# Kernel optimization log

Measured on AMD Instinct MI355X. Metric: run time of the kernel, lower is better.

Reference implementation:

```python
import jax, jax.numpy as jnp
from jax import lax
import numpy as np

T = 65536   # seq_len (one long utterance)
C = 8       # n_cgs (contour generators in graph)
F = 10      # n_features + n_context
H = 64      # GRU hidden size
NIN = 4     # rnn_inputs=None -> x_module[:, 1:5]
NOUT = 1    # n_output


def setup_inputs() -> dict:
    key = jax.random.key(0)
    ks = jax.random.split(key, 9)
    x = jax.random.normal(ks[0], (T, F, C), jnp.float32)
    cg_masks = jnp.ones((T, C), jnp.int32)
    contour_starts = jax.random.randint(ks[1], (T, C), 0, 2, jnp.int32)
    # first timestep of each cg must start a contour (original loop only
    # produces output from the first start onward)
    contour_starts = contour_starts.at[0].set(1)
    s = 1.0 / np.sqrt(H)
    u = lambda k, shp: jax.random.uniform(k, shp, jnp.float32, -s, s)
    W_ih = u(ks[2], (C, 3 * H, NIN))
    W_hh = u(ks[3], (C, 3 * H, H))
    b_ih = u(ks[4], (C, 3 * H))
    b_hh = u(ks[5], (C, 3 * H))
    W_out = u(ks[6], (C, NOUT, H))
    b_out = u(ks[7], (C, NOUT))
    return {"x": x, "cg_masks": cg_masks, "contour_starts": contour_starts,
            "W_ih": W_ih, "W_hh": W_hh, "b_ih": b_ih, "b_hh": b_hh,
            "W_out": W_out, "b_out": b_out}


def reference(x, cg_masks, contour_starts, W_ih, W_hh, b_ih, b_hh, W_out, b_out):
    # x: (T, F, C); select rnn input features 1:5 for every contour generator
    x4 = x[:, 1:5, :]                                   # (T, 4, C)
    # precompute input-to-hidden gates for all cgs at once: (T, C, 3H)
    gx = jnp.einsum('tfc,cgf->tcg', x4, W_ih) + b_ih
    starts = contour_starts == 1                        # (T, C) bool

    def step(h, inp):
        gx_t, start_t = inp                             # (C, 3H), (C,)
        # ragged segment boundary -> reset hidden state (h_module = None)
        h = jnp.where(start_t[:, None], jnp.zeros_like(h), h)
        gh = jnp.einsum('cgh,ch->cg', W_hh, h) + b_hh   # (C, 3H)
        r = jax.nn.sigmoid(gx_t[:, :H] + gh[:, :H])
        z = jax.nn.sigmoid(gx_t[:, H:2 * H] + gh[:, H:2 * H])
        n = jnp.tanh(gx_t[:, 2 * H:] + r * gh[:, 2 * H:])
        h_new = (1.0 - z) * n + z * h
        return h_new, h_new

    h0 = jnp.zeros((C, H), x.dtype)
    _, hs = lax.scan(step, h0, (gx, starts))            # hs: (T, C, H)
    out = jnp.einsum('tch,coh->tco', hs, W_out) + b_out  # (T, C, NOUT)
    # scatter-add of each segment's y_rnn into y; with all-ones masks the
    # segments tile [0, T) so this is the masked sum over contour generators
    active = (cg_masks == 1).astype(out.dtype)[..., None]  # (T, C, 1)
    y = jnp.sum(out * active, axis=1)                   # (T, NOUT)
    return y
```

## Files before the change

kernel.cpp:

```cpp
#include <hip/hip_runtime.h>

#define T_LEN 65536
#define C_CH 8
#define CLEN 16
#define NB 16
#define WIN (CLEN * NB)
#define NBLK 2048
#define SCANW 6
#define MAXB 32

typedef short bf16x8 __attribute__((ext_vector_type(8)));
typedef float f32x4 __attribute__((ext_vector_type(4)));
typedef unsigned int uint;
typedef uint u32x4 __attribute__((ext_vector_type(4)));
typedef unsigned long long u64;

#define MFMA32 __builtin_amdgcn_mfma_f32_16x16x32_bf16

#define SC_RZ 1.4426950408889634f
#define SC_N  2.8853900817779268f

__device__ __forceinline__ uint f2bf(float f) {
    uint u = __float_as_uint(f);
    return (u + 0x7FFFu + ((u >> 16) & 1u)) >> 16;
}
__device__ __forceinline__ uint pk(float a, float b) {
    return f2bf(a) | (f2bf(b) << 16);
}
__device__ __forceinline__ uint cvtpk(float lo, float hi) {
    uint r;
    asm("v_cvt_pk_bf16_f32 %0, %1, %2" : "=v"(r) : "v"(lo), "v"(hi));
    return r;
}
__device__ __forceinline__ float expneg(float x) { return __builtin_amdgcn_exp2f(-x); }
__device__ __forceinline__ bf16x8 mk8(uint a, uint b, uint c, uint d) {
    union { uint u[4]; bf16x8 v; } x;
    x.u[0] = a; x.u[1] = b; x.u[2] = c; x.u[3] = d;
    return x.v;
}
__device__ __forceinline__ bf16x8 q2b(u32x4 q) {
    union { u32x4 q; bf16x8 b; } u; u.q = q; return u.b;
}
__device__ __forceinline__ float rcpf(float v) { return __builtin_amdgcn_rcpf(v); }

__global__ __launch_bounds__(64, 2) void gru_mfma(
    const float* __restrict__ x,
    const int*   __restrict__ cg,
    const int*   __restrict__ cs,
    const float* __restrict__ W_ih,
    const float* __restrict__ W_hh,
    const float* __restrict__ b_ih,
    const float* __restrict__ b_hh,
    const float* __restrict__ W_out,
    const float* __restrict__ b_out,
    float* __restrict__ y)
{
    __shared__ u64 stw[SCANW], acw[SCANW];
    __shared__ int sb[NB + 1];
    __shared__ float yw[NB][MAXB + 1];
    __shared__ uint2 bxl[MAXB][NB];

    const int lane = threadIdx.x;
    const int l15 = lane & 15, l4 = lane >> 4;
    const int slot = blockIdx.x & 7;
    const int c    = (blockIdx.x >> 3) & 7;
    const int whi  = blockIdx.x >> 6;
    const int w    = whi * 8 + slot;
    const int RB   = w * WIN;

    for (int rr = 0; rr < SCANW; ++rr) {
        int t = RB + rr * 64 + lane;
        int sv = 0, av = 0;
        if (t < T_LEN) { sv = cs[t * C_CH + c]; av = cg[t * C_CH + c]; }
        u64 m1 = __ballot(sv == 1);
        u64 m2 = __ballot(av == 1);
        if (lane == 0) { stw[rr] = m1; acw[rr] = m2; }
    }
    __syncthreads();

    if (lane <= NB) {
        int rel = lane * CLEN;
        int q = rel >> 6, r0 = rel & 63;
        u64 m = stw[q] >> r0;
        int pos = -1;
        if (m) pos = rel + __ffsll(m) - 1;
        else {
            for (int q2 = q + 1; q2 < SCANW; ++q2)
                if (stw[q2]) { pos = (q2 << 6) + __ffsll(stw[q2]) - 1; break; }
        }
        int Sa;
        if (pos >= 0) Sa = RB + pos;
        else {
            int t = RB + SCANW * 64;
            while (t < T_LEN && cs[t * C_CH + c] != 1) ++t;
            Sa = t;
        }
        sb[lane] = min(Sa, T_LEN);
    }
    __syncthreads();

    const int S = sb[l15];
    const int len = sb[l15 + 1] - S;
    int Lmax = len;
#pragma unroll
    for (int o = 1; o < 16; o <<= 1) Lmax = max(Lmax, __shfl_xor(Lmax, o));

    const float* Wc = W_hh + c * 192 * 64;
    u32x4 AhA[12][2];
#pragma unroll
    for (int tm = 0; tm < 12; ++tm) {
        const float sc = (tm < 8) ? SC_RZ : SC_N;
#pragma unroll
        for (int kt = 0; kt < 2; ++kt) {
            const float* p = Wc + (16 * tm + l15) * 64 + 32 * kt + 4 * l4;
            float4 a = *(const float4*)p;
            float4 b = *(const float4*)(p + 16);
            AhA[tm][kt] = (u32x4){ pk(a.x * sc, a.y * sc), pk(a.z * sc, a.w * sc),
                                   pk(b.x * sc, b.y * sc), pk(b.z * sc, b.w * sc) };
            asm volatile("" : "+a"(AhA[tm][kt]));
        }
    }
    u32x4 WoA[2];
#pragma unroll
    for (int kt = 0; kt < 2; ++kt) {
        uint d0 = 0, d1 = 0, d2 = 0, d3 = 0;
        if (l15 == 0) {
            const float* wp = W_out + c * 64 + 32 * kt + 4 * l4;
            d0 = pk(wp[0], wp[1]);  d1 = pk(wp[2], wp[3]);
            d2 = pk(wp[16], wp[17]); d3 = pk(wp[18], wp[19]);
        }
        WoA[kt] = (u32x4){ d0, d1, d2, d3 };
        asm volatile("" : "+a"(WoA[kt]));
    }

    uint Axd[12][2];
#pragma unroll
    for (int tm = 0; tm < 12; ++tm) {
        const float sc = (tm < 8) ? SC_RZ : SC_N;
        int row = 16 * tm + l15;
        uint d0 = 0, d1 = 0;
        if (l4 == 0) {
            float4 wi4 = *(const float4*)(W_ih + (c * 192 + row) * 4);
            d0 = pk(wi4.x * sc, wi4.y * sc);
            d1 = pk(wi4.z * sc, wi4.w * sc);
        } else if (l4 == 1) {
            float bias = (tm < 8) ? (b_ih[c * 192 + row] + b_hh[c * 192 + row]) * SC_RZ
                                  : b_ih[c * 192 + row] * SC_N;
            d0 = f2bf(bias);
        }
        Axd[tm][0] = d0; Axd[tm][1] = d1;
    }
    f32x4 bhn4[4];
#pragma unroll
    for (int tn = 0; tn < 4; ++tn) {
        float4 v = *(const float4*)(b_hh + c * 192 + 128 + 16 * tn + 4 * l4);
        bhn4[tn] = (f32x4){v.x * SC_N, v.y * SC_N, v.z * SC_N, v.w * SC_N};
    }
    const float bo = b_out[c];

    uint B0[4], B1[4];
#pragma unroll
    for (int i = 0; i < 4; ++i) { B0[i] = 0u; B1[i] = 0u; }
    const uint bx_c0 = (l4 == 1) ? 0x00003F80u : 0u;
    const f32x4 z4 = {0.f, 0.f, 0.f, 0.f};

    for (int s0 = 0; s0 < Lmax; s0 += MAXB) {
        const int Lb = min(MAXB, Lmax - s0);

        const int npair = Lb * NB;
        for (int p = lane; p < npair; p += 64) {
            int s = p >> 4;
            int t = min(sb[p & 15] + s0 + s, T_LEN - 1);
            const float* xp = x + (size_t)t * 80 + 8 + c;
            bxl[s][p & 15] = make_uint2(pk(xp[0], xp[8]), pk(xp[16], xp[24]));
        }
        int off = (S - RB) + s0;
        int q = off >> 6, r0 = off & 63;
        u64 w0s = (q < SCANW) ? stw[q] : 0ull;
        u64 w1s = (q + 1 < SCANW) ? stw[q + 1] : 0ull;
        u64 ms = (w0s >> r0) | (r0 ? (w1s << (64 - r0)) : 0ull);
        __syncthreads();

        for (int s = 0; s < Lb; ++s) {
            const bool rst = (ms >> s) & 1;
#pragma unroll
            for (int i = 0; i < 4; ++i) {
                B0[i] = rst ? 0u : B0[i];
                B1[i] = rst ? 0u : B1[i];
            }

            uint2 bx = bxl[s][l15];
            const bf16x8 Bx  = mk8((lane < 16) ? bx.x : bx_c0,
                                   (lane < 16) ? bx.y : 0u, 0u, 0u);
            const bf16x8 Bh0 = mk8(B0[0], B0[1], B0[2], B0[3]);
            const bf16x8 Bh1 = mk8(B1[0], B1[1], B1[2], B1[3]);

            uint nB[8];
#pragma unroll
            for (int tm = 0; tm < 4; ++tm) {
                const int tz = tm + 4, tn = tm + 8;
                f32x4 ar = MFMA32(mk8(Axd[tm][0], Axd[tm][1], 0u, 0u), Bx, z4, 0, 0, 0);
                ar = MFMA32(q2b(AhA[tm][0]), Bh0, ar, 0, 0, 0);
                ar = MFMA32(q2b(AhA[tm][1]), Bh1, ar, 0, 0, 0);
                f32x4 az = MFMA32(mk8(Axd[tz][0], Axd[tz][1], 0u, 0u), Bx, z4, 0, 0, 0);
                az = MFMA32(q2b(AhA[tz][0]), Bh0, az, 0, 0, 0);
                az = MFMA32(q2b(AhA[tz][1]), Bh1, az, 0, 0, 0);
                f32x4 gx = MFMA32(mk8(Axd[tn][0], Axd[tn][1], 0u, 0u), Bx, z4, 0, 0, 0);
                f32x4 gh = MFMA32(q2b(AhA[tn][0]), Bh0, bhn4[tm], 0, 0, 0);
                gh = MFMA32(q2b(AhA[tn][1]), Bh1, gh, 0, 0, 0);

                float hv[4];
#pragma unroll
                for (int i = 0; i < 4; ++i) {
                    float rr = rcpf(1.f + expneg(ar[i]));
                    float zz = rcpf(1.f + expneg(az[i]));
                    float np2 = fmaf(rr, gh[i], gx[i]);
                    float nn = fmaf(2.f, rcpf(1.f + expneg(np2)), -1.f);
                    const uint bd = (tm < 2) ? B0[2 * (tm & 1) + (i >> 1)]
                                             : B1[2 * (tm & 1) + (i >> 1)];
                    const float hold = __uint_as_float((i & 1) ? (bd & 0xFFFF0000u)
                                                               : (bd << 16));
                    float hh = fmaf(zz, hold - nn, nn);
                    hv[i] = hh;
                }
                nB[2 * tm]     = cvtpk(hv[0], hv[1]);
                nB[2 * tm + 1] = cvtpk(hv[2], hv[3]);
            }
            B0[0] = nB[0]; B0[1] = nB[1]; B0[2] = nB[2]; B0[3] = nB[3];
            B1[0] = nB[4]; B1[1] = nB[5]; B1[2] = nB[6]; B1[3] = nB[7];

            const bf16x8 Bh0n = mk8(B0[0], B0[1], B0[2], B0[3]);
            const bf16x8 Bh1n = mk8(B1[0], B1[1], B1[2], B1[3]);
            f32x4 y4 = MFMA32(q2b(WoA[0]), Bh0n, z4, 0, 0, 0);
            y4 = MFMA32(q2b(WoA[1]), Bh1n, y4, 0, 0, 0);
            if (lane < 16 && (s0 + s) < len) yw[lane][s] = y4[0];
        }
        __syncthreads();

        for (int b = 0; b < NB; ++b) {
            int Sb = sb[b];
            int lenb = sb[b + 1] - Sb;
            int sg = s0 + lane;
            if (lane < Lb && sg < lenb) {
                int offa = (Sb - RB) + sg;
                int qa = offa >> 6;
                bool act;
                if (qa < SCANW) act = (acw[qa] >> (offa & 63)) & 1;
                else            act = cg[(Sb + sg) * C_CH + c] == 1;
                if (act) atomicAdd(&y[Sb + sg], yw[b][lane] + bo);
            }
        }
        __syncthreads();
    }
}

extern "C" void kernel_launch(void* const* d_in, const int* in_sizes, int n_in,
                              void* d_out, int out_size, void* d_ws, size_t ws_size,
                              hipStream_t stream) {
    const float* x     = (const float*)d_in[0];
    const int*   cg    = (const int*)  d_in[1];
    const int*   cs    = (const int*)  d_in[2];
    const float* W_ih  = (const float*)d_in[3];
    const float* W_hh  = (const float*)d_in[4];
    const float* b_ih  = (const float*)d_in[5];
    const float* b_hh  = (const float*)d_in[6];
    const float* W_out = (const float*)d_in[7];
    const float* b_out = (const float*)d_in[8];
    float* y = (float*)d_out;

    hipMemsetAsync(y, 0, (size_t)out_size * sizeof(float), stream);
    gru_mfma<<<NBLK, 64, 0, stream>>>(x, cg, cs, W_ih, W_hh, b_ih, b_hh,
                                      W_out, b_out, y);
}
```

Measured before the change: 81.42 us.

## Split MFMA accumulation chains, prefetch next-step input, raise wave priority

The recurrent step's three dependent MFMA chains per gate are each split into two independent partial accumulators that are summed in VALU, which shortens the serial MFMA dependency on the critical path. The next timestep's packed input is loaded from LDS one iteration ahead, so its latency is off the step's critical path. The step body is also wrapped in s_setprio so these waves get issue priority over others on the same SIMD. In exchange there are extra VALU adds and live registers, and rounding order changes slightly.

```diff
diff --git a/kernel.cpp b/kernel.cpp
--- a/kernel.cpp
+++ b/kernel.cpp
@@ -181,7 +181,13 @@
         u64 ms = (w0s >> r0) | (r0 ? (w1s << (64 - r0)) : 0ull);
         __syncthreads();
 
+        uint2 bxn = bxl[0][l15];
+
         for (int s = 0; s < Lb; ++s) {
+            __builtin_amdgcn_s_setprio(1);
+            const uint2 bxc = bxn;
+            if (s + 1 < Lb) bxn = bxl[s + 1][l15];
+
             const bool rst = (ms >> s) & 1;
 #pragma unroll
             for (int i = 0; i < 4; ++i) {
@@ -189,9 +195,8 @@
                 B1[i] = rst ? 0u : B1[i];
             }
 
-            uint2 bx = bxl[s][l15];
-            const bf16x8 Bx  = mk8((lane < 16) ? bx.x : bx_c0,
-                                   (lane < 16) ? bx.y : 0u, 0u, 0u);
+            const bf16x8 Bx  = mk8((lane < 16) ? bxc.x : bx_c0,
+                                   (lane < 16) ? bxc.y : 0u, 0u, 0u);
             const bf16x8 Bh0 = mk8(B0[0], B0[1], B0[2], B0[3]);
             const bf16x8 Bh1 = mk8(B1[0], B1[1], B1[2], B1[3]);
 
@@ -199,22 +204,22 @@
 #pragma unroll
             for (int tm = 0; tm < 4; ++tm) {
                 const int tz = tm + 4, tn = tm + 8;
-                f32x4 ar = MFMA32(mk8(Axd[tm][0], Axd[tm][1], 0u, 0u), Bx, z4, 0, 0, 0);
-                ar = MFMA32(q2b(AhA[tm][0]), Bh0, ar, 0, 0, 0);
-                ar = MFMA32(q2b(AhA[tm][1]), Bh1, ar, 0, 0, 0);
-                f32x4 az = MFMA32(mk8(Axd[tz][0], Axd[tz][1], 0u, 0u), Bx, z4, 0, 0, 0);
-                az = MFMA32(q2b(AhA[tz][0]), Bh0, az, 0, 0, 0);
-                az = MFMA32(q2b(AhA[tz][1]), Bh1, az, 0, 0, 0);
-                f32x4 gx = MFMA32(mk8(Axd[tn][0], Axd[tn][1], 0u, 0u), Bx, z4, 0, 0, 0);
-                f32x4 gh = MFMA32(q2b(AhA[tn][0]), Bh0, bhn4[tm], 0, 0, 0);
-                gh = MFMA32(q2b(AhA[tn][1]), Bh1, gh, 0, 0, 0);
+                f32x4 arx = MFMA32(mk8(Axd[tm][0], Axd[tm][1], 0u, 0u), Bx, z4, 0, 0, 0);
+                f32x4 aru = MFMA32(q2b(AhA[tm][0]), Bh0, arx, 0, 0, 0);
+                f32x4 arv = MFMA32(q2b(AhA[tm][1]), Bh1, z4, 0, 0, 0);
+                f32x4 azx = MFMA32(mk8(Axd[tz][0], Axd[tz][1], 0u, 0u), Bx, z4, 0, 0, 0);
+                f32x4 azu = MFMA32(q2b(AhA[tz][0]), Bh0, azx, 0, 0, 0);
+                f32x4 azv = MFMA32(q2b(AhA[tz][1]), Bh1, z4, 0, 0, 0);
+                f32x4 gx  = MFMA32(mk8(Axd[tn][0], Axd[tn][1], 0u, 0u), Bx, z4, 0, 0, 0);
+                f32x4 ghu = MFMA32(q2b(AhA[tn][0]), Bh0, bhn4[tm], 0, 0, 0);
+                f32x4 ghv = MFMA32(q2b(AhA[tn][1]), Bh1, z4, 0, 0, 0);
 
                 float hv[4];
 #pragma unroll
                 for (int i = 0; i < 4; ++i) {
-                    float rr = rcpf(1.f + expneg(ar[i]));
-                    float zz = rcpf(1.f + expneg(az[i]));
-                    float np2 = fmaf(rr, gh[i], gx[i]);
+                    float rr = rcpf(1.f + expneg(aru[i] + arv[i]));
+                    float zz = rcpf(1.f + expneg(azu[i] + azv[i]));
+                    float np2 = fmaf(rr, ghu[i] + ghv[i], gx[i]);
                     float nn = fmaf(2.f, rcpf(1.f + expneg(np2)), -1.f);
                     const uint bd = (tm < 2) ? B0[2 * (tm & 1) + (i >> 1)]
                                              : B1[2 * (tm & 1) + (i >> 1)];
@@ -233,6 +238,7 @@
             const bf16x8 Bh1n = mk8(B1[0], B1[1], B1[2], B1[3]);
             f32x4 y4 = MFMA32(q2b(WoA[0]), Bh0n, z4, 0, 0, 0);
             y4 = MFMA32(q2b(WoA[1]), Bh1n, y4, 0, 0, 0);
+            __builtin_amdgcn_s_setprio(0);
             if (lane < 16 && (s0 + s) < len) yw[lane][s] = y4[0];
         }
         __syncthreads();
```

After: 89.94 us. +10.5%, slower.
